# Kernel optimization log

Measured on AMD Instinct MI355X. Metric: run time of the kernel, lower is better.

The kernel has to match this reference:

```python
import jax, jax.numpy as jnp
import numpy as np

IN_CH = 256
MED_CH = IN_CH // 2


def setup_inputs() -> dict:
    key = jax.random.key(0)
    ks = jax.random.split(key, 9)
    B, C, H, W = 16, IN_CH, 64, 64
    s = 1.0 / np.sqrt(C)
    sm = 1.0 / np.sqrt(MED_CH)
    return {
        "x": jax.random.normal(ks[0], (B, C, H, W), dtype=jnp.float32),
        "w_o": jax.random.normal(ks[1], (MED_CH, C), dtype=jnp.float32) * s,
        "b_o": jax.random.normal(ks[2], (MED_CH,), dtype=jnp.float32) * 0.01,
        "w_v": jax.random.normal(ks[3], (MED_CH, C), dtype=jnp.float32) * s,
        "b_v": jax.random.normal(ks[4], (MED_CH,), dtype=jnp.float32) * 0.01,
        "w_c": jax.random.normal(ks[5], (C, MED_CH), dtype=jnp.float32) * sm,
        "b_c": jax.random.normal(ks[6], (C,), dtype=jnp.float32) * 0.01,
        "gamma": jax.random.normal(ks[7], (1,), dtype=jnp.float32) * 0.1,
    }


def reference(x, w_o, b_o, w_v, b_v, w_c, b_c, gamma):
    B, C, H, W = x.shape
    N = H * W
    xf = x.reshape(B, C, N)  # [B,C,N]
    # 1x1 convs == per-pixel linear projections
    o = jnp.einsum("mc,bcn->bmn", w_o, xf) + b_o[None, :, None]   # [B,M,N]
    v = jnp.einsum("mc,bcn->bmn", w_v, xf) + b_v[None, :, None]   # [B,M,N]
    x_o = o.transpose(0, 2, 1)                                     # [B,N,M]
    x_v = jax.nn.softmax(v, axis=-1)                               # softmax over N
    # NOTE: original code reuses conv_v for the 's' branch (conv_s unused)
    x_s = jax.nn.softmax(v.transpose(0, 2, 1), axis=-1)            # [B,N,M], softmax over M
    A = jnp.einsum("bmn,bnk->bmk", x_v, x_s)                       # [B,M,M]
    Bt = jnp.einsum("bnm,bmk->bnk", x_o, A).transpose(0, 2, 1)     # [B,M,N]
    out = jax.nn.relu(jnp.einsum("cm,bmn->bcn", w_c, Bt) + b_c[None, :, None])
    result = gamma[0] * out.reshape(B, C, H, W) + x
    return result
```

## Files before the change

### kernel.cpp

```cpp
#include <hip/hip_runtime.h>
#include <math.h>

constexpr int Bn = 16;
constexpr int Cn = 256;
constexpr int Mn = 128;
constexpr int Nn = 4096;

typedef short bf16x8 __attribute__((ext_vector_type(8)));
typedef float f32x4 __attribute__((ext_vector_type(4)));
typedef unsigned short us8 __attribute__((ext_vector_type(8)));
typedef unsigned short us4 __attribute__((ext_vector_type(4)));

static __device__ __forceinline__ unsigned short f2bf(float f) {
  union { float f; unsigned int u; } c{f};
  unsigned int u = c.u;
  u += 0x7FFFu + ((u >> 16) & 1u);
  return (unsigned short)(u >> 16);
}

static __device__ __forceinline__ void gload_lds16(const void* g, void* l) {
  __builtin_amdgcn_global_load_lds(
      (const __attribute__((address_space(1))) unsigned int*)g,
      (__attribute__((address_space(3))) unsigned int*)l, 16, 0, 0);
}

__global__ __launch_bounds__(256) void k_prep(
    const float* __restrict__ x, unsigned short* __restrict__ xT,
    const float* __restrict__ w_o, const float* __restrict__ w_v,
    unsigned short* __restrict__ Wv, unsigned short* __restrict__ woT,
    float* __restrict__ rs) {
  const int b = blockIdx.z;
  const int c0 = blockIdx.y * 128;
  const int n0 = blockIdx.x * 64;
  const int t = threadIdx.x;

  if (blockIdx.y == 0 && blockIdx.z == 0) {
    int idx = blockIdx.x * 256 + t;
    if (idx < Bn * Mn) rs[idx] = 0.f;
    if (idx < 8192) {
      int row = idx >> 6;
      int c4 = (idx & 63) * 4;
      float4 f = *(const float4*)&w_v[(size_t)row * Cn + c4];
      us4 g = {f2bf(f.x), f2bf(f.y), f2bf(f.z), f2bf(f.w)};
      *(us4*)&Wv[(size_t)row * Cn + c4] = g;
    } else {
      int j = idx - 8192;
      int cp = j >> 5;
      int m4 = (j & 31) * 4;
      us4 g;
#pragma unroll
      for (int e = 0; e < 4; ++e) g[e] = f2bf(w_o[(size_t)(m4 + e) * Cn + cp]);
      *(us4*)&woT[(size_t)cp * Mn + m4] = g;
    }
  }

  const int n4 = (t & 15) * 4;
  const int c8 = c0 + (t >> 4) * 8;
  const float* xb = x + ((size_t)b * Cn + c8) * Nn + n0 + n4;
  float4 r[8];
#pragma unroll
  for (int i = 0; i < 8; ++i) r[i] = *(const float4*)&xb[(size_t)i * Nn];
  unsigned short* dst = xT + ((size_t)b * Nn + n0 + n4) * Cn + c8;
#pragma unroll
  for (int j = 0; j < 4; ++j) {
    us8 g;
#pragma unroll
    for (int i = 0; i < 8; ++i) g[i] = f2bf(((const float*)&r[i])[j]);
    *(us8*)&dst[(size_t)j * Cn] = g;
  }
}

__global__ __launch_bounds__(256) void k_proj_v(
    const unsigned short* __restrict__ Wv,
    const unsigned short* __restrict__ xT,
    const float* __restrict__ b_v,
    float* __restrict__ Ap, float* __restrict__ rs) {
  __shared__ us8 pool[16 * 128 * 2];
  __shared__ float cs_lds[4][128];
  unsigned short* ldsA = (unsigned short*)pool;
  unsigned short* ldsB = (unsigned short*)pool + 8 * 128 * 8;
  const int b = blockIdx.y;
  const int nt = blockIdx.x;
  const int t = threadIdx.x;
  const int wave = t >> 6, lane = t & 63;
  const int quad = lane >> 4, l16 = lane & 15;
  const int wm = (wave & 1) * 64, wn = (wave >> 1) * 64;
  f32x4 acc[4][4] = {};
  const unsigned short* xb = xT + ((size_t)b * Nn + nt * 128) * Cn;
  const int rowS = t & 127;
  const int gS = t >> 7;

  uint4 rB[4];
#pragma unroll
  for (int p = 0; p < 4; ++p)
    rB[p] = *(const uint4*)&xb[(size_t)rowS * Cn + (p * 2 + gS) * 8];

  for (int k0 = 0; k0 < Cn; k0 += 64) {
#pragma unroll
    for (int p = 0; p < 4; ++p) {
      int s = p * 256 + t;
      *(uint4*)&ldsB[(size_t)s * 8] = rB[p];
      gload_lds16(&Wv[(size_t)rowS * Cn + k0 + (p * 2 + gS) * 8],
                  &ldsA[(size_t)s * 8]);
    }
    __syncthreads();
    if (k0 + 64 < Cn) {
#pragma unroll
      for (int p = 0; p < 4; ++p)
        rB[p] = *(const uint4*)&xb[(size_t)rowS * Cn + k0 + 64 + (p * 2 + gS) * 8];
    }
#pragma unroll
    for (int s = 0; s < 2; ++s) {
      bf16x8 af[4], bfr[4];
#pragma unroll
      for (int i = 0; i < 4; ++i)
        af[i] = *(const bf16x8*)&ldsA[(size_t)((s * 4 + quad) * 128 + wm + i * 16 + l16) * 8];
#pragma unroll
      for (int j = 0; j < 4; ++j)
        bfr[j] = *(const bf16x8*)&ldsB[(size_t)((s * 4 + quad) * 128 + wn + j * 16 + l16) * 8];
#pragma unroll
      for (int i = 0; i < 4; ++i)
#pragma unroll
        for (int j = 0; j < 4; ++j)
          acc[i][j] = __builtin_amdgcn_mfma_f32_16x16x32_bf16(af[i], bfr[j], acc[i][j], 0, 0, 0);
    }
    __syncthreads();
  }

#pragma unroll
  for (int i = 0; i < 4; ++i) {
#pragma unroll
    for (int r = 0; r < 4; ++r) {
      float bi = b_v[wm + i * 16 + quad * 4 + r];
#pragma unroll
      for (int j = 0; j < 4; ++j)
        acc[i][j][r] = __expf(acc[i][j][r] + bi);
    }
  }

#pragma unroll
  for (int i = 0; i < 4; ++i) {
#pragma unroll
    for (int r = 0; r < 4; ++r) {
      float s = acc[i][0][r] + acc[i][1][r] + acc[i][2][r] + acc[i][3][r];
      s += __shfl_xor(s, 1); s += __shfl_xor(s, 2);
      s += __shfl_xor(s, 4); s += __shfl_xor(s, 8);
      if (l16 == 0)
        atomicAdd(&rs[b * Mn + wm + i * 16 + quad * 4 + r], s);
    }
  }

  float csj[4];
#pragma unroll
  for (int j = 0; j < 4; ++j) {
    float c = 0.f;
#pragma unroll
    for (int i = 0; i < 4; ++i)
#pragma unroll
      for (int r = 0; r < 4; ++r) c += acc[i][j][r];
    c += __shfl_xor(c, 16);
    c += __shfl_xor(c, 32);
    csj[j] = c;
  }
  if (quad == 0) {
#pragma unroll
    for (int j = 0; j < 4; ++j) cs_lds[wave][wn + j * 16 + l16] = csj[j];
  }
  __syncthreads();

  const int cbase = (wave >> 1) * 2;
  float rinv[4];
#pragma unroll
  for (int j = 0; j < 4; ++j) {
    int nl = wn + j * 16 + l16;
    rinv[j] = rsqrtf(cs_lds[cbase][nl] + cs_lds[cbase + 1][nl]);
  }

  unsigned short* Hs = (unsigned short*)pool;
  unsigned short* Ls = Hs + 16 * 128 * 8;
#pragma unroll
  for (int i = 0; i < 4; ++i) {
#pragma unroll
    for (int r = 0; r < 4; ++r) {
      int m = wm + i * 16 + quad * 4 + r;
#pragma unroll
      for (int j = 0; j < 4; ++j) {
        int nl = wn + j * 16 + l16;
        float u = acc[i][j][r] * rinv[j];
        unsigned short h = f2bf(u);
        union { unsigned int q; float f; } hf{(unsigned int)h << 16};
        int idx = ((nl >> 3) * 128 + (m ^ (nl >> 3))) * 8 + (nl & 7);
        Hs[idx] = h;
        Ls[idx] = f2bf(u - hf.f);
      }
    }
  }
  __syncthreads();

  const bf16x8* Hv = (const bf16x8*)pool;
  const bf16x8* Lv = Hv + 16 * 128;
#pragma unroll
  for (int i = 0; i < 4; ++i)
#pragma unroll
    for (int j = 0; j < 4; ++j) acc[i][j] = (f32x4){0.f, 0.f, 0.f, 0.f};
#pragma unroll
  for (int s = 0; s < 4; ++s) {
    int g = s * 4 + quad;
    bf16x8 hA[4], lA[4], hB[4], lB[4];
#pragma unroll
    for (int i = 0; i < 4; ++i) {
      int mi = wm + i * 16 + l16;
      int ki = wn + i * 16 + l16;
      hA[i] = Hv[g * 128 + (mi ^ g)];
      lA[i] = Lv[g * 128 + (mi ^ g)];
      hB[i] = Hv[g * 128 + (ki ^ g)];
      lB[i] = Lv[g * 128 + (ki ^ g)];
    }
#pragma unroll
    for (int i = 0; i < 4; ++i)
#pragma unroll
      for (int j = 0; j < 4; ++j) {
        acc[i][j] = __builtin_amdgcn_mfma_f32_16x16x32_bf16(hA[i], hB[j], acc[i][j], 0, 0, 0);
        acc[i][j] = __builtin_amdgcn_mfma_f32_16x16x32_bf16(hA[i], lB[j], acc[i][j], 0, 0, 0);
        acc[i][j] = __builtin_amdgcn_mfma_f32_16x16x32_bf16(lA[i], hB[j], acc[i][j], 0, 0, 0);
      }
  }

  float* Apb = Ap + ((size_t)nt * Bn + b) * (Mn * Mn);
#pragma unroll
  for (int i = 0; i < 4; ++i) {
#pragma unroll
    for (int r = 0; r < 4; ++r) {
      int m = wm + i * 16 + quad * 4 + r;
      float* row = &Apb[(size_t)m * Mn];
#pragma unroll
      for (int j = 0; j < 4; ++j)
        row[wn + j * 16 + l16] = acc[i][j][r];
    }
  }
}

__global__ __launch_bounds__(256) void k_reduceA(
    const float* __restrict__ Ap, const float* __restrict__ rs,
    float* __restrict__ A, int S) {
  int tid = blockIdx.x * 256 + threadIdx.x;
  int idx4 = tid * 4;
  int b = idx4 / (Mn * Mn);
  int off = idx4 - b * (Mn * Mn);
  float4 s = {0.f, 0.f, 0.f, 0.f};
  for (int s0 = 0; s0 < S; ++s0) {
    float4 p = *(const float4*)&Ap[((size_t)s0 * Bn + b) * (Mn * Mn) + off];
    s.x += p.x; s.y += p.y; s.z += p.z; s.w += p.w;
  }
  float sc = 1.0f / rs[b * Mn + (off >> 7)];
  s.x *= sc; s.y *= sc; s.z *= sc; s.w *= sc;
  *(float4*)&A[idx4] = s;
}

__global__ __launch_bounds__(256) void k_w2(
    const float* __restrict__ w_c, const float* __restrict__ A,
    unsigned short* __restrict__ W2bf) {
  __shared__ float As[64][68];
  __shared__ float wcs[64][68];
  const int b = blockIdx.z;
  const int m0 = blockIdx.x * 64;
  const int c0 = blockIdx.y * 64;
  const int t = threadIdx.x;
  const int tc = (t >> 4) * 4, tmm = (t & 15) * 4;
  float acc[4][4] = {};
  for (int k0 = 0; k0 < Mn; k0 += 64) {
    int r = t >> 2;
    int k4 = (t & 3) * 4;
#pragma unroll
    for (int p = 0; p < 4; ++p) {
      int k = k4 + p * 16;
      float4 a4 = *(const float4*)&A[((size_t)(b * Mn + m0 + r)) * Mn + k0 + k];
      As[k + 0][r] = a4.x; As[k + 1][r] = a4.y; As[k + 2][r] = a4.z; As[k + 3][r] = a4.w;
      float4 w4 = *(const float4*)&w_c[(size_t)(c0 + r) * Mn + k0 + k];
      wcs[k + 0][r] = w4.x; wcs[k + 1][r] = w4.y; wcs[k + 2][r] = w4.z; wcs[k + 3][r] = w4.w;
    }
    __syncthreads();
#pragma unroll
    for (int kk = 0; kk < 64; ++kk) {
      float4 w4 = *(const float4*)&wcs[kk][tc];
      float4 a4 = *(const float4*)&As[kk][tmm];
      float w[4] = {w4.x, w4.y, w4.z, w4.w};
      float a[4] = {a4.x, a4.y, a4.z, a4.w};
#pragma unroll
      for (int i = 0; i < 4; ++i)
#pragma unroll
        for (int jj = 0; jj < 4; ++jj) acc[i][jj] = fmaf(w[i], a[jj], acc[i][jj]);
    }
    __syncthreads();
  }
#pragma unroll
  for (int i = 0; i < 4; ++i) {
    us4 g4 = {f2bf(acc[i][0]), f2bf(acc[i][1]), f2bf(acc[i][2]), f2bf(acc[i][3])};
    *(us4*)&W2bf[((size_t)(b * Cn + c0 + tc + i)) * Mn + m0 + tmm] = g4;
  }
}

__global__ __launch_bounds__(256) void k_ww(
    const unsigned short* __restrict__ W2bf, const unsigned short* __restrict__ woT,
    const float* __restrict__ b_o, const float* __restrict__ b_c,
    unsigned short* __restrict__ WW, float* __restrict__ bb) {
  __shared__ us8 ldsA[128 * 16];
  __shared__ us8 ldsB[128 * 16];
  __shared__ float bo_lds[128];
  const int b = blockIdx.z;
  const int c_t = blockIdx.y * 128;
  const int cp_t = blockIdx.x * 128;
  const int t = threadIdx.x;
  const int wave = t >> 6, lane = t & 63;
  const int quad = lane >> 4, l16 = lane & 15;
  const int wc = (wave & 1) * 64, wp = (wave >> 1) * 64;
  const unsigned short* W2b = W2bf + ((size_t)b * Cn + c_t) * Mn;
  const unsigned short* woB = woT + (size_t)cp_t * Mn;

#pragma unroll
  for (int p = 0; p < 8; ++p) {
    int s = p * 256 + t;
    int row = s >> 4, g = s & 15;
    int slot = row * 16 + (g ^ (row & 15));
    ldsA[slot] = *(const us8*)&W2b[(size_t)row * Mn + g * 8];
    ldsB[slot] = *(const us8*)&woB[(size_t)row * Mn + g * 8];
  }
  if (blockIdx.x == 0 && t < 128) bo_lds[t] = b_o[t];
  __syncthreads();

  f32x4 acc[4][4] = {};
#pragma unroll
  for (int s = 0; s < 4; ++s) {
    int gq = s * 4 + quad;
    int xo = gq ^ l16;
    bf16x8 af[4], bfr[4];
#pragma unroll
    for (int i = 0; i < 4; ++i)
      af[i] = *(const bf16x8*)&ldsA[(wc + i * 16 + l16) * 16 + xo];
#pragma unroll
    for (int j = 0; j < 4; ++j)
      bfr[j] = *(const bf16x8*)&ldsB[(wp + j * 16 + l16) * 16 + xo];
#pragma unroll
    for (int i = 0; i < 4; ++i)
#pragma unroll
      for (int j = 0; j < 4; ++j)
        acc[i][j] = __builtin_amdgcn_mfma_f32_16x16x32_bf16(af[i], bfr[j], acc[i][j], 0, 0, 0);
  }

#pragma unroll
  for (int i = 0; i < 4; ++i) {
#pragma unroll
    for (int r = 0; r < 4; ++r) {
      int c = c_t + wc + i * 16 + quad * 4 + r;
      unsigned short* row = &WW[((size_t)b * Cn + c) * Cn + cp_t];
#pragma unroll
      for (int j = 0; j < 4; ++j)
        row[wp + j * 16 + l16] = f2bf(acc[i][j][r]);
    }
  }

  if (blockIdx.x == 0 && t < 128) {
    float s = 0.f;
#pragma unroll
    for (int g = 0; g < 16; ++g) {
      us8 h = ldsA[t * 16 + (g ^ (t & 15))];
#pragma unroll
      for (int e = 0; e < 8; ++e) {
        union { unsigned int u; float f; } cv{(unsigned int)h[e] << 16};
        s = fmaf(cv.f, bo_lds[g * 8 + e], s);
      }
    }
    bb[b * Cn + c_t + t] = s + b_c[c_t + t];
  }
}

__global__ __launch_bounds__(256) void k_final_mfma(
    const unsigned short* __restrict__ WW, const unsigned short* __restrict__ xT,
    const float* __restrict__ x, const float* __restrict__ bb,
    const float* __restrict__ gamma, float* __restrict__ out) {
  __shared__ us8 ldsA[128 * 16];
  __shared__ us8 ldsB[128 * 16];
  const int flat = blockIdx.x + 32 * blockIdx.y + 64 * (int)blockIdx.z;
  const int swz = (flat & 7) * 128 + (flat >> 3);
  const int n_t = (swz & 31) * 128;
  const int c_t = ((swz >> 5) & 1) * 128;
  const int b = swz >> 6;
  const int t = threadIdx.x;
  const int wave = t >> 6, lane = t & 63;
  const int quad = lane >> 4, l16 = lane & 15;
  const int wc = (wave & 1) * 64, wn = (wave >> 1) * 64;
  const unsigned short* WWb = WW + ((size_t)b * Cn + c_t) * Cn;
  const unsigned short* xTb = xT + ((size_t)b * Nn + n_t) * Cn;
  unsigned short* ldsAu = (unsigned short*)ldsA;
  unsigned short* ldsBu = (unsigned short*)ldsB;

  f32x4 acc[4][4] = {};
  for (int k0 = 0; k0 < Cn; k0 += 128) {
#pragma unroll
    for (int p = 0; p < 8; ++p) {
      int s = p * 256 + t;
      int row = s >> 4, g = s & 15;
      int gsw = g ^ (row & 15);
      gload_lds16(&WWb[(size_t)row * Cn + k0 + gsw * 8], &ldsAu[(size_t)s * 8]);
      gload_lds16(&xTb[(size_t)row * Cn + k0 + gsw * 8], &ldsBu[(size_t)s * 8]);
    }
    __syncthreads();
#pragma unroll
    for (int s = 0; s < 4; ++s) {
      int gq = s * 4 + quad;
      int xo = gq ^ l16;
      bf16x8 af[4], bfr[4];
#pragma unroll
      for (int i = 0; i < 4; ++i)
        af[i] = *(const bf16x8*)&ldsA[(wc + i * 16 + l16) * 16 + xo];
#pragma unroll
      for (int j = 0; j < 4; ++j)
        bfr[j] = *(const bf16x8*)&ldsB[(wn + j * 16 + l16) * 16 + xo];
#pragma unroll
      for (int i = 0; i < 4; ++i)
#pragma unroll
        for (int j = 0; j < 4; ++j)
          acc[i][j] = __builtin_amdgcn_mfma_f32_16x16x32_bf16(af[i], bfr[j], acc[i][j], 0, 0, 0);
    }
    __syncthreads();
  }

  float g = gamma[0];
#pragma unroll
  for (int i = 0; i < 4; ++i) {
#pragma unroll
    for (int r = 0; r < 4; ++r) {
      int c = c_t + wc + i * 16 + quad * 4 + r;
      float bias = bb[b * Cn + c];
      const float* xr = &x[((size_t)b * Cn + c) * Nn + n_t];
      float* orow = &out[((size_t)b * Cn + c) * Nn + n_t];
#pragma unroll
      for (int j = 0; j < 4; ++j) {
        int n = wn + j * 16 + l16;
        orow[n] = g * fmaxf(acc[i][j][r] + bias, 0.f) + xr[n];
      }
    }
  }
}

extern "C" void kernel_launch(void* const* d_in, const int* in_sizes, int n_in,
                              void* d_out, int out_size, void* d_ws, size_t ws_size,
                              hipStream_t stream) {
  const float* x   = (const float*)d_in[0];
  const float* w_o = (const float*)d_in[1];
  const float* b_o = (const float*)d_in[2];
  const float* w_v = (const float*)d_in[3];
  const float* b_v = (const float*)d_in[4];
  const float* w_c = (const float*)d_in[5];
  const float* b_c = (const float*)d_in[6];
  const float* gm  = (const float*)d_in[7];

  constexpr int S = Nn / 128;
  float* ws = (float*)d_ws;
  float* rs = ws;
  float* bb = rs + Bn * Mn;
  float* A  = bb + Bn * Cn;
  float* Ap = A + (size_t)Bn * Mn * Mn;
  unsigned short* WW   = (unsigned short*)(Ap + (size_t)S * Bn * Mn * Mn);
  unsigned short* W2bf = WW + (size_t)Bn * Cn * Cn;
  unsigned short* xT   = W2bf + (size_t)Bn * Cn * Mn;
  unsigned short* Wv   = xT + (size_t)Bn * Nn * Cn;
  unsigned short* woT  = Wv + (size_t)Mn * Cn;

  k_prep<<<dim3(Nn / 64, 2, Bn), 256, 0, stream>>>(x, xT, w_o, w_v, Wv, woT, rs);
  k_proj_v<<<dim3(Nn / 128, Bn), 256, 0, stream>>>(Wv, xT, b_v, Ap, rs);
  k_reduceA<<<dim3(Bn * Mn * Mn / 1024), 256, 0, stream>>>(Ap, rs, A, S);
  k_w2<<<dim3(Mn / 64, Cn / 64, Bn), 256, 0, stream>>>(w_c, A, W2bf);
  k_ww<<<dim3(2, 2, Bn), 256, 0, stream>>>(W2bf, woT, b_o, b_c, WW, bb);
  k_final_mfma<<<dim3(Nn / 128, Cn / 128, Bn), 256, 0, stream>>>(WW, xT, x, bb, gm, (float*)d_out);
}
```

Measured before the change: 205.8 us.

## Replace partial-A buffer and reduce kernel with atomic accumulation into A

The projection kernel now atomically adds its per-tile A contributions directly into a single per-batch A buffer that k_prep zeroes. This removes the large split-partial buffer and the separate reduction kernel, with normalization by row sums moved into k_w2. It also raises wave priority around MFMA loops. The trade-off is many contended float atomics and nondeterministic summation order.

```diff
diff --git a/kernel.cpp b/kernel.cpp
--- a/kernel.cpp
+++ b/kernel.cpp
@@ -28,7 +28,7 @@
     const float* __restrict__ x, unsigned short* __restrict__ xT,
     const float* __restrict__ w_o, const float* __restrict__ w_v,
     unsigned short* __restrict__ Wv, unsigned short* __restrict__ woT,
-    float* __restrict__ rs) {
+    float* __restrict__ rs, float* __restrict__ A) {
   const int b = blockIdx.z;
   const int c0 = blockIdx.y * 128;
   const int n0 = blockIdx.x * 64;
@@ -37,6 +37,9 @@
   if (blockIdx.y == 0 && blockIdx.z == 0) {
     int idx = blockIdx.x * 256 + t;
     if (idx < Bn * Mn) rs[idx] = 0.f;
+    float4 z = {0.f, 0.f, 0.f, 0.f};
+    float4* Az = (float4*)A + (size_t)idx * 4;
+    Az[0] = z; Az[1] = z; Az[2] = z; Az[3] = z;
     if (idx < 8192) {
       int row = idx >> 6;
       int c4 = (idx & 63) * 4;
@@ -74,7 +77,7 @@
     const unsigned short* __restrict__ Wv,
     const unsigned short* __restrict__ xT,
     const float* __restrict__ b_v,
-    float* __restrict__ Ap, float* __restrict__ rs) {
+    float* __restrict__ A, float* __restrict__ rs) {
   __shared__ us8 pool[16 * 128 * 2];
   __shared__ float cs_lds[4][128];
   unsigned short* ldsA = (unsigned short*)pool;
@@ -109,6 +112,7 @@
       for (int p = 0; p < 4; ++p)
         rB[p] = *(const uint4*)&xb[(size_t)rowS * Cn + k0 + 64 + (p * 2 + gS) * 8];
     }
+    __builtin_amdgcn_s_setprio(1);
 #pragma unroll
     for (int s = 0; s < 2; ++s) {
       bf16x8 af[4], bfr[4];
@@ -124,6 +128,7 @@
         for (int j = 0; j < 4; ++j)
           acc[i][j] = __builtin_amdgcn_mfma_f32_16x16x32_bf16(af[i], bfr[j], acc[i][j], 0, 0, 0);
     }
+    __builtin_amdgcn_s_setprio(0);
     __syncthreads();
   }
 
@@ -203,6 +208,7 @@
   for (int i = 0; i < 4; ++i)
 #pragma unroll
     for (int j = 0; j < 4; ++j) acc[i][j] = (f32x4){0.f, 0.f, 0.f, 0.f};
+  __builtin_amdgcn_s_setprio(1);
 #pragma unroll
   for (int s = 0; s < 4; ++s) {
     int g = s * 4 + quad;
@@ -225,41 +231,25 @@
         acc[i][j] = __builtin_amdgcn_mfma_f32_16x16x32_bf16(lA[i], hB[j], acc[i][j], 0, 0, 0);
       }
   }
-
-  float* Apb = Ap + ((size_t)nt * Bn + b) * (Mn * Mn);
+  __builtin_amdgcn_s_setprio(0);
+
+  float* Ab = A + (size_t)b * Mn * Mn;
 #pragma unroll
   for (int i = 0; i < 4; ++i) {
 #pragma unroll
     for (int r = 0; r < 4; ++r) {
       int m = wm + i * 16 + quad * 4 + r;
-      float* row = &Apb[(size_t)m * Mn];
-#pragma unroll
-      for (int j = 0; j < 4; ++j)
-        row[wn + j * 16 + l16] = acc[i][j][r];
-    }
-  }
-}
-
-__global__ __launch_bounds__(256) void k_reduceA(
-    const float* __restrict__ Ap, const float* __restrict__ rs,
-    float* __restrict__ A, int S) {
-  int tid = blockIdx.x * 256 + threadIdx.x;
-  int idx4 = tid * 4;
-  int b = idx4 / (Mn * Mn);
-  int off = idx4 - b * (Mn * Mn);
-  float4 s = {0.f, 0.f, 0.f, 0.f};
-  for (int s0 = 0; s0 < S; ++s0) {
-    float4 p = *(const float4*)&Ap[((size_t)s0 * Bn + b) * (Mn * Mn) + off];
-    s.x += p.x; s.y += p.y; s.z += p.z; s.w += p.w;
-  }
-  float sc = 1.0f / rs[b * Mn + (off >> 7)];
-  s.x *= sc; s.y *= sc; s.z *= sc; s.w *= sc;
-  *(float4*)&A[idx4] = s;
+      float* row = &Ab[(size_t)m * Mn];
+#pragma unroll
+      for (int j = 0; j < 4; ++j)
+        atomicAdd(&row[wn + j * 16 + l16], acc[i][j][r]);
+    }
+  }
 }
 
 __global__ __launch_bounds__(256) void k_w2(
     const float* __restrict__ w_c, const float* __restrict__ A,
-    unsigned short* __restrict__ W2bf) {
+    const float* __restrict__ rs, unsigned short* __restrict__ W2bf) {
   __shared__ float As[64][68];
   __shared__ float wcs[64][68];
   const int b = blockIdx.z;
@@ -267,15 +257,17 @@
   const int c0 = blockIdx.y * 64;
   const int t = threadIdx.x;
   const int tc = (t >> 4) * 4, tmm = (t & 15) * 4;
+  const int r = t >> 2;
+  const int k4 = (t & 3) * 4;
+  const float irs = 1.0f / rs[b * Mn + m0 + r];
   float acc[4][4] = {};
   for (int k0 = 0; k0 < Mn; k0 += 64) {
-    int r = t >> 2;
-    int k4 = (t & 3) * 4;
 #pragma unroll
     for (int p = 0; p < 4; ++p) {
       int k = k4 + p * 16;
       float4 a4 = *(const float4*)&A[((size_t)(b * Mn + m0 + r)) * Mn + k0 + k];
-      As[k + 0][r] = a4.x; As[k + 1][r] = a4.y; As[k + 2][r] = a4.z; As[k + 3][r] = a4.w;
+      As[k + 0][r] = a4.x * irs; As[k + 1][r] = a4.y * irs;
+      As[k + 2][r] = a4.z * irs; As[k + 3][r] = a4.w * irs;
       float4 w4 = *(const float4*)&w_c[(size_t)(c0 + r) * Mn + k0 + k];
       wcs[k + 0][r] = w4.x; wcs[k + 1][r] = w4.y; wcs[k + 2][r] = w4.z; wcs[k + 3][r] = w4.w;
     }
@@ -455,22 +447,19 @@
   const float* b_c = (const float*)d_in[6];
   const float* gm  = (const float*)d_in[7];
 
-  constexpr int S = Nn / 128;
   float* ws = (float*)d_ws;
   float* rs = ws;
   float* bb = rs + Bn * Mn;
   float* A  = bb + Bn * Cn;
-  float* Ap = A + (size_t)Bn * Mn * Mn;
-  unsigned short* WW   = (unsigned short*)(Ap + (size_t)S * Bn * Mn * Mn);
+  unsigned short* WW   = (unsigned short*)(A + (size_t)Bn * Mn * Mn);
   unsigned short* W2bf = WW + (size_t)Bn * Cn * Cn;
   unsigned short* xT   = W2bf + (size_t)Bn * Cn * Mn;
   unsigned short* Wv   = xT + (size_t)Bn * Nn * Cn;
   unsigned short* woT  = Wv + (size_t)Mn * Cn;
 
-  k_prep<<<dim3(Nn / 64, 2, Bn), 256, 0, stream>>>(x, xT, w_o, w_v, Wv, woT, rs);
-  k_proj_v<<<dim3(Nn / 128, Bn), 256, 0, stream>>>(Wv, xT, b_v, Ap, rs);
-  k_reduceA<<<dim3(Bn * Mn * Mn / 1024), 256, 0, stream>>>(Ap, rs, A, S);
-  k_w2<<<dim3(Mn / 64, Cn / 64, Bn), 256, 0, stream>>>(w_c, A, W2bf);
+  k_prep<<<dim3(Nn / 64, 2, Bn), 256, 0, stream>>>(x, xT, w_o, w_v, Wv, woT, rs, A);
+  k_proj_v<<<dim3(Nn / 128, Bn), 256, 0, stream>>>(Wv, xT, b_v, A, rs);
+  k_w2<<<dim3(Mn / 64, Cn / 64, Bn), 256, 0, stream>>>(w_c, A, rs, W2bf);
   k_ww<<<dim3(2, 2, Bn), 256, 0, stream>>>(W2bf, woT, b_o, b_c, WW, bb);
   k_final_mfma<<<dim3(Nn / 128, Cn / 128, Bn), 256, 0, stream>>>(WW, xT, x, bb, gm, (float*)d_out);
 }
```

After: 222.7 us. +8.2%, slower.
